# Kernel tuning notes

Measured on AMD Instinct MI355X. Metric: run time of the kernel, lower is better.

## Reference

```python
import jax, jax.numpy as jnp
import numpy as np

# Model dims (match init_kwargs)
N_HEADS = 32
N_KV_HEADS = 8
DIM = 4096
HEAD_DIM = DIM // N_HEADS  # 128
N_REP = N_HEADS // N_KV_HEADS  # 4
MAX_SEQ_LEN = 2048
THETA = 10000.0


def precompute_freqs(dim, end, theta=THETA):
    inv = 1.0 / (theta ** (jnp.arange(0, dim, 2, dtype=jnp.float32) / dim))  # [dim/2]
    t = jnp.arange(end, dtype=jnp.float32)
    f = jnp.outer(t, inv)  # [end, dim/2]
    return jnp.cos(f), jnp.sin(f)


def apply_rope(x, cos, sin):
    # x: [b, s, h, d]; cos/sin: [s, d/2]. Pairs (x[...,2i], x[...,2i+1]) form complex numbers.
    xr = x[..., 0::2]
    xi = x[..., 1::2]
    c = cos[None, :, None, :]
    s = sin[None, :, None, :]
    out_r = xr * c - xi * s
    out_i = xr * s + xi * c
    return jnp.stack([out_r, out_i], axis=-1).reshape(x.shape)


def setup_inputs() -> dict:
    key = jax.random.key(0)
    ks = jax.random.split(key, 5)
    B, S = 4, 1024
    x = jax.random.normal(ks[0], (B, S, DIM), dtype=jnp.float32)
    wq = jax.random.normal(ks[1], (DIM, N_HEADS * HEAD_DIM), dtype=jnp.float32) * 0.02
    wk = jax.random.normal(ks[2], (DIM, N_KV_HEADS * HEAD_DIM), dtype=jnp.float32) * 0.02
    wv = jax.random.normal(ks[3], (DIM, N_KV_HEADS * HEAD_DIM), dtype=jnp.float32) * 0.02
    wo = jax.random.normal(ks[4], (N_HEADS * HEAD_DIM, DIM), dtype=jnp.float32) * 0.02
    # causal mask, additive: 0 on/below diagonal, -1e9 above
    mask = jnp.where(jnp.tril(jnp.ones((S, S), dtype=bool)), 0.0, -1e9).astype(jnp.float32)[None, None]
    return {"x": x, "wq": wq, "wk": wk, "wv": wv, "wo": wo, "mask": mask, "start_pos": 0}


def reference(x, wq, wk, wv, wo, mask, start_pos):
    B, S, _ = x.shape
    # QKV projections
    xq = (x @ wq).reshape(B, S, N_HEADS, HEAD_DIM)
    xk = (x @ wk).reshape(B, S, N_KV_HEADS, HEAD_DIM)
    xv = (x @ wv).reshape(B, S, N_KV_HEADS, HEAD_DIM)
    # RoPE on q, k at positions [start_pos, start_pos+S)
    cos, sin = precompute_freqs(HEAD_DIM, MAX_SEQ_LEN * 2)
    cos_s = jax.lax.dynamic_slice_in_dim(cos, start_pos, S, 0)
    sin_s = jax.lax.dynamic_slice_in_dim(sin, start_pos, S, 0)
    xq = apply_rope(xq, cos_s, sin_s)
    xk = apply_rope(xk, cos_s, sin_s)
    # KV-cache scatter-update (cache starts zeroed), then read prefix
    cache_k = jnp.zeros((B, MAX_SEQ_LEN, N_KV_HEADS, HEAD_DIM), dtype=x.dtype)
    cache_v = jnp.zeros_like(cache_k)
    cache_k = jax.lax.dynamic_update_slice(cache_k, xk, (0, start_pos, 0, 0))
    cache_v = jax.lax.dynamic_update_slice(cache_v, xv, (0, start_pos, 0, 0))
    kv_len = start_pos + S
    keys = cache_k[:, :kv_len]    # [b, kv_len, n_kv, d]
    values = cache_v[:, :kv_len]
    # GQA without materializing repeated KV: split q heads into (kv_group, rep)
    q = xq.reshape(B, S, N_KV_HEADS, N_REP, HEAD_DIM)
    scale = 1.0 / jnp.sqrt(jnp.float32(HEAD_DIM)).astype(x.dtype)
    scores = jnp.einsum('bsgrd,btgd->bgrst', q, keys) * scale  # [b, g, r, s, t]
    scores = scores + mask.reshape(1, 1, 1, S, kv_len)
    probs = jax.nn.softmax(scores, axis=-1)
    out = jnp.einsum('bgrst,btgd->bsgrd', probs, values)  # [b, s, g, r, d]
    out = out.reshape(B, S, N_HEADS * HEAD_DIM)
    return out @ wo
```

## Files before the change

kernel.cpp:

```cpp
#include <hip/hip_runtime.h>
#include <hip/hip_bf16.h>
#include <stdint.h>

typedef __bf16 bf16raw;
typedef __attribute__((ext_vector_type(8))) __bf16 bf16x8;
typedef __attribute__((ext_vector_type(4))) float f32x4;

#define DIMD 4096
#define NHEAD 32
#define NKVH 8
#define HD 128
#define SEQ 1024
#define NB 4
#define NTOK 4096
#define NQKV 6144

__device__ __forceinline__ void gload_lds16(const void* gsrc, void* ldst) {
  __builtin_amdgcn_global_load_lds(
      (const __attribute__((address_space(1))) void*)gsrc,
      (__attribute__((address_space(3))) void*)ldst, 16, 0, 0);
}

__global__ void cast_f32_bf16_kernel(const float* __restrict__ src,
                                     __hip_bfloat16* __restrict__ dst, int n) {
  int i = (blockIdx.x * 256 + threadIdx.x) * 8;
  if (i >= n) return;
  f32x4 a = *(const f32x4*)(src + i);
  f32x4 b = *(const f32x4*)(src + i + 4);
  union { bf16x8 v; __hip_bfloat16 e[8]; } o;
#pragma unroll
  for (int j = 0; j < 4; ++j) {
    o.e[j] = __float2bfloat16(a[j]);
    o.e[4 + j] = __float2bfloat16(b[j]);
  }
  *(bf16x8*)(dst + i) = o.v;
}

__global__ void transpose_cast_kernel(const float* __restrict__ src,
                                      __hip_bfloat16* __restrict__ dst,
                                      int K, int N) {
  __shared__ float tile[32][33];
  int n0 = blockIdx.x * 32, k0 = blockIdx.y * 32;
  int tx = threadIdx.x, ty = threadIdx.y;
#pragma unroll
  for (int i = 0; i < 4; ++i)
    tile[ty + 8 * i][tx] = src[(size_t)(k0 + ty + 8 * i) * N + n0 + tx];
  __syncthreads();
#pragma unroll
  for (int i = 0; i < 4; ++i)
    dst[(size_t)(n0 + ty + 8 * i) * K + k0 + tx] =
        __float2bfloat16(tile[tx][ty + 8 * i]);
}

__global__ void rope_table_kernel(float* __restrict__ cosb, float* __restrict__ sinb) {
  int idx = blockIdx.x * 256 + threadIdx.x;
  int s = idx >> 6, j = idx & 63;
  float inv = 1.0f / powf(10000.0f, (float)(2 * j) * (1.0f / 128.0f));
  float ang = (float)s * inv;
  cosb[idx] = cosf(ang);
  sinb[idx] = sinf(ang);
}


#define LGSB()                                       \
  asm volatile("s_waitcnt lgkmcnt(0)" ::: "memory"); \
  __builtin_amdgcn_sched_barrier(0)

#define QMFMA(AFR, BFR, MB, NB)                                            \
  _Pragma("unroll") for (int mf2 = 0; mf2 < 4; ++mf2)                      \
  _Pragma("unroll") for (int nf2 = 0; nf2 < 2; ++nf2)                      \
  _Pragma("unroll") for (int kk2 = 0; kk2 < 2; ++kk2)                      \
      acc[(MB) + mf2][(NB) + nf2] = __builtin_amdgcn_mfma_f32_16x16x32_bf16( \
          AFR[mf2 * 2 + kk2], BFR[nf2 * 2 + kk2], acc[(MB) + mf2][(NB) + nf2], 0, 0, 0)

#define TILE4(BUF, ST1, ST2, ST3, ST4, VM)                        \
  {                                                               \
    _Pragma("unroll") for (int mf = 0; mf < 4; ++mf)              \
    _Pragma("unroll") for (int kk = 0; kk < 2; ++kk)              \
        alo[mf * 2 + kk] = ldsA(BUF, mf, kk);                     \
    _Pragma("unroll") for (int nf = 0; nf < 2; ++nf)              \
    _Pragma("unroll") for (int kk = 0; kk < 2; ++kk)              \
        bq[nf * 2 + kk] = ldsB(BUF, nf, kk);                      \
    ST1;                                                          \
    LGSB();                                                       \
    __builtin_amdgcn_s_setprio(1);                                \
    QMFMA(alo, bq, 0, 0);                                         \
    __builtin_amdgcn_s_setprio(0);                                \
    _Pragma("unroll") for (int mf = 0; mf < 4; ++mf)              \
    _Pragma("unroll") for (int kk = 0; kk < 2; ++kk)              \
        ahi[mf * 2 + kk] = ldsA(BUF, mf + 4, kk);                 \
    ST2;                                                          \
    LGSB();                                                       \
    __builtin_amdgcn_s_setprio(1);                                \
    QMFMA(ahi, bq, 4, 0);                                         \
    __builtin_amdgcn_s_setprio(0);                                \
    _Pragma("unroll") for (int nf = 0; nf < 2; ++nf)              \
    _Pragma("unroll") for (int kk = 0; kk < 2; ++kk)              \
        bq[nf * 2 + kk] = ldsB(BUF, nf + 2, kk);                  \
    LGSB();                                                       \
    __builtin_amdgcn_s_setprio(1);                                \
    QMFMA(alo, bq, 0, 2);                                         \
    __builtin_amdgcn_s_setprio(0);                                \
    __builtin_amdgcn_s_barrier();   \
    ST3;                                                          \
    ST4;                                                          \
    __builtin_amdgcn_s_setprio(1);                                \
    QMFMA(ahi, bq, 4, 2);                                         \
    __builtin_amdgcn_s_setprio(0);                                \
    VM;                                                           \
    __builtin_amdgcn_s_barrier();   \
  }

template <typename OutT, bool ROPE>
__global__ __launch_bounds__(512, 2) void gemm256_kernel(
    const __hip_bfloat16* __restrict__ A, const __hip_bfloat16* __restrict__ BT,
    OutT* __restrict__ C, int M, int N, int K,
    const float* __restrict__ cosb, const float* __restrict__ sinb,
    __hip_bfloat16* __restrict__ vtc) {
  __shared__ __align__(16) char lds_[131072];
  const int tid = threadIdx.x;
  const int w = tid >> 6, l = tid & 63;
  const int lr = l & 15, lk = l >> 4;
  const int wm = w >> 2, wn = w & 3;

  const int nbn = N >> 8;
  const int nwg = (M >> 8) * nbn;
  const int cpx = nwg >> 3;
  const int bid = blockIdx.x;
  const int swz = (bid & 7) * cpx + (bid >> 3);
  const int m0 = (swz / nbn) << 8;
  const int n0 = (swz % nbn) << 8;

  const size_t Kb = (size_t)K * 2;
  const char* Ab = (const char*)A + (size_t)m0 * Kb;
  const char* Bb = (const char*)BT + (size_t)n0 * Kb;
  const int srcb = ((l & 7) ^ (l >> 3)) * 16;
  const int crow = l >> 3;

  auto stageA = [&](int buf, int half, int kt) {
#pragma unroll
    for (int j = 0; j < 2; ++j) {
      int row = half * 128 + (w * 2 + j) * 8 + crow;
      gload_lds16(Ab + (size_t)row * Kb + (size_t)kt * 128 + srcb,
                  lds_ + buf * 65536 + half * 16384 + (w * 2 + j) * 1024);
    }
  };
  auto stageB = [&](int buf, int half, int kt) {
#pragma unroll
    for (int j = 0; j < 2; ++j) {
      int row = half * 128 + (w * 2 + j) * 8 + crow;
      gload_lds16(Bb + (size_t)row * Kb + (size_t)kt * 128 + srcb,
                  lds_ + buf * 65536 + 32768 + half * 16384 + (w * 2 + j) * 1024);
    }
  };
  auto ldsA = [&](int buf, int mf, int kk) {
    int rih = mf * 16 + lr;
    int cb = (kk * 64 + lk * 16) ^ ((lr & 7) << 4);
    return *(const bf16x8*)(lds_ + buf * 65536 + wm * 16384 + rih * 128 + cb);
  };
  auto ldsB = [&](int buf, int nf, int kk) {
    int rih = (wn & 1) * 64 + nf * 16 + lr;
    int cb = (kk * 64 + lk * 16) ^ ((lr & 7) << 4);
    return *(const bf16x8*)(lds_ + buf * 65536 + 32768 + (wn >> 1) * 16384 +
                            rih * 128 + cb);
  };

  f32x4 acc[8][4] = {};
  bf16x8 alo[8], ahi[8], bq[4];

  stageA(0, 0, 0);
  stageA(0, 1, 0);
  stageB(0, 0, 0);
  stageB(0, 1, 0);
  stageA(1, 0, 1);
  stageA(1, 1, 1);
  asm volatile("s_waitcnt vmcnt(4)" ::: "memory");
  __builtin_amdgcn_s_barrier();

  const int NT = K >> 6;
  for (int E = 0; E < NT - 2; E += 2) {
    TILE4(0, stageB(1, 0, E + 1), stageB(1, 1, E + 1),
          stageA(0, 0, E + 2), stageA(0, 1, E + 2),
          asm volatile("s_waitcnt vmcnt(4)" ::: "memory"));
    TILE4(1, stageB(0, 0, E + 2), stageB(0, 1, E + 2),
          stageA(1, 0, E + 3), stageA(1, 1, E + 3),
          asm volatile("s_waitcnt vmcnt(4)" ::: "memory"));
  }
  TILE4(0, stageB(1, 0, NT - 1), stageB(1, 1, NT - 1), (void)0, (void)0,
        asm volatile("s_waitcnt vmcnt(0)" ::: "memory"));
  TILE4(1, (void)0, (void)0, (void)0, (void)0, (void)0);

#pragma unroll
  for (int mf = 0; mf < 8; ++mf) {
    int row = m0 + wm * 128 + mf * 16 + lk * 4;
#pragma unroll
    for (int nf = 0; nf < 4; ++nf) {
      int colb = n0 + wn * 64 + nf * 16;
      f32x4 v = acc[mf][nf];
      if constexpr (ROPE) {
        if (colb < 5120) {
          int d = (colb & 127) + lr;
          int jj = d >> 1;
          bool even = (d & 1) == 0;
#pragma unroll
          for (int j = 0; j < 4; ++j) {
            float p = __shfl_xor(v[j], 1);
            int s = (row + j) & (SEQ - 1);
            float c = cosb[s * 64 + jj];
            float sn = sinb[s * 64 + jj];
            v[j] = even ? (v[j] * c - p * sn) : (p * sn + v[j] * c);
          }
        } else {
          int col = colb + lr;
          int d = col & 127;
          int hk = (col >> 7) & 7;
          int b = row >> 10;
          int s = row & (SEQ - 1);
          union { uint64_t u; __hip_bfloat16 e[4]; } pk;
#pragma unroll
          for (int j = 0; j < 4; ++j) pk.e[j] = __float2bfloat16(v[j]);
          size_t off = ((size_t)((b * 8 + hk) * 16 + (s >> 6)) * 128 + d) * 64 +
                       (s & 63);
          *(uint64_t*)(vtc + off) = pk.u;
          continue;
        }
      }
#pragma unroll
      for (int j = 0; j < 4; ++j) {
        size_t off = (size_t)(row + j) * N + colb + lr;
        if constexpr (sizeof(OutT) == 2)
          C[off] = __float2bfloat16(v[j]);
        else
          C[off] = v[j];
      }
    }
  }
}

__global__ __launch_bounds__(256, 2) void attn_kernel(
    const __hip_bfloat16* __restrict__ qkv,
    const __hip_bfloat16* __restrict__ vtc,
    __hip_bfloat16* __restrict__ out) {
  __shared__ __align__(16) char Ks[2][16384];
  __shared__ __align__(16) char Vs[2][16384];
  __shared__ __align__(16) char Ps[4][2048];

  const int tid = threadIdx.x;
  const int w = tid >> 6, l = tid & 63;
  const int lr = l & 15, lk = l >> 4;
  const int bx = blockIdx.x;
  const int pair = bx >> 7;
  const int hb = bx & 127;
  const int h = hb & 31;
  const int b = hb >> 5;
  const int hk = h >> 2;

  const char* KgB = (const char*)qkv +
                    ((size_t)(b * SEQ) * NQKV + DIMD + hk * HD) * 2;
  const char* VgB = (const char*)vtc + (size_t)(b * NKVH + hk) * (16 * 16384);
  char* Pw = &Ps[w][0];

  const float cs = 0.12752039889171495f;
  const float ebias = 11.541560327111707f;

  auto stageK = [&](int buf, int kvb) {
#pragma unroll
    for (int j = 0; j < 4; ++j) {
      int i = w * 4 + j;
      int row = i * 4 + (l >> 4);
      int si = ((l & 15) * 16) ^ ((row & 7) << 4);
      gload_lds16(KgB + (size_t)(kvb + row) * (NQKV * 2) + si,
                  &Ks[buf][i * 1024]);
    }
  };
  auto stageV = [&](int buf, int t) {
#pragma unroll
    for (int j = 0; j < 4; ++j) {
      int i = w * 4 + j;
      int row = i * 8 + (l >> 3);
      int si = ((l & 7) * 16) ^ ((row & 7) << 4);
      gload_lds16(VgB + (size_t)t * 16384 + row * 128 + si,
                  &Vs[buf][i * 1024]);
    }
  };

  for (int qsel = 0; qsel < 2; ++qsel) {
    const int qtile = qsel ? (15 - pair) : pair;
    const int qbase = qtile * 64 + w * 16;
    const int nkv = qtile + 1;

    const __hip_bfloat16* Qp =
        qkv + (size_t)(b * SEQ + qbase + lr) * NQKV + h * HD + lk * 8;
    bf16x8 aq[4];
#pragma unroll
    for (int ks = 0; ks < 4; ++ks) aq[ks] = *(const bf16x8*)(Qp + ks * 32);

    f32x4 O[8] = {};
    float lsum[4] = {0.f, 0.f, 0.f, 0.f};

    stageK(0, 0);
    stageV(0, 0);
    asm volatile("s_waitcnt vmcnt(0)" ::: "memory");
    __syncthreads();

    for (int t = 0; t < nkv; ++t) {
      const int cur = t & 1;
      if (t + 1 < nkv) {
        stageK(cur ^ 1, (t + 1) * 64);
        stageV(cur ^ 1, t + 1);
      }
      const int kvb = t * 64;

      f32x4 st[4] = {};
      __builtin_amdgcn_s_setprio(1);
#pragma unroll
      for (int nt = 0; nt < 4; ++nt) {
        int row = nt * 16 + lr;
        const char* kr = &Ks[cur][row * 256];
        int sw = (row & 7) << 4;
#pragma unroll
        for (int ks = 0; ks < 4; ++ks) {
          bf16x8 bk = *(const bf16x8*)(kr + ((ks * 64 + lk * 16) ^ sw));
          st[nt] = __builtin_amdgcn_mfma_f32_16x16x32_bf16(aq[ks], bk, st[nt], 0, 0, 0);
        }
      }
      __builtin_amdgcn_s_setprio(0);

      const bool needmask = (kvb + 63 > qbase);
#pragma unroll
      for (int j = 0; j < 4; ++j) {
        int qrow = qbase + lk * 4 + j;
        int prow = lk * 4 + j;
        int sw = (prow & 7) << 4;
#pragma unroll
        for (int nt = 0; nt < 4; ++nt) {
          float p = exp2f(fmaf(st[nt][j], cs, -ebias));
          if (needmask && (kvb + nt * 16 + lr > qrow)) p = 0.f;
          lsum[j] += p;
          *(__hip_bfloat16*)(Pw + prow * 128 + (((nt * 16 + lr) * 2) ^ sw)) =
              __float2bfloat16(p);
        }
      }

      asm volatile("s_waitcnt lgkmcnt(0)" ::: "memory");
      __builtin_amdgcn_sched_barrier(0);

      __builtin_amdgcn_s_setprio(1);
#pragma unroll
      for (int ks = 0; ks < 2; ++ks) {
        bf16x8 ap = *(const bf16x8*)(Pw + lr * 128 +
                                     ((ks * 64 + lk * 16) ^ ((lr & 7) << 4)));
#pragma unroll
        for (int dt = 0; dt < 8; ++dt) {
          int row = dt * 16 + lr;
          bf16x8 bv = *(const bf16x8*)(&Vs[cur][row * 128 +
                                               ((ks * 64 + lk * 16) ^ ((row & 7) << 4))]);
          O[dt] = __builtin_amdgcn_mfma_f32_16x16x32_bf16(ap, bv, O[dt], 0, 0, 0);
        }
      }
      __builtin_amdgcn_s_setprio(0);

      __syncthreads();
    }

#pragma unroll
    for (int j = 0; j < 4; ++j) {
      float rs = lsum[j];
      rs += __shfl_xor(rs, 1);
      rs += __shfl_xor(rs, 2);
      rs += __shfl_xor(rs, 4);
      rs += __shfl_xor(rs, 8);
      float inv = 1.0f / rs;
      __hip_bfloat16* orow =
          out + (size_t)(b * SEQ + qbase + lk * 4 + j) * DIMD + h * HD;
#pragma unroll
      for (int dt = 0; dt < 8; ++dt)
        orow[dt * 16 + lr] = __float2bfloat16(O[dt][j] * inv);
    }
  }
}

extern "C" void kernel_launch(void* const* d_in, const int* in_sizes, int n_in,
                              void* d_out, int out_size, void* d_ws, size_t ws_size,
                              hipStream_t stream) {
  const float* x = (const float*)d_in[0];
  const float* wq = (const float*)d_in[1];
  const float* wk = (const float*)d_in[2];
  const float* wv = (const float*)d_in[3];
  const float* wo = (const float*)d_in[4];
  float* out = (float*)d_out;

  char* ws = (char*)d_ws;
  const size_t MB = 1024 * 1024;
  __hip_bfloat16* xb = (__hip_bfloat16*)(ws);
  __hip_bfloat16* wqkvt = (__hip_bfloat16*)(ws + 32 * MB);
  __hip_bfloat16* wot = (__hip_bfloat16*)(ws + 80 * MB);
  __hip_bfloat16* qkv = (__hip_bfloat16*)(ws + 112 * MB);
  __hip_bfloat16* vtc = (__hip_bfloat16*)(ws + 160 * MB);
  float* cosb = (float*)(ws + 168 * MB);
  float* sinb = cosb + SEQ * 64;

  cast_f32_bf16_kernel<<<NTOK * DIMD / 8 / 256, 256, 0, stream>>>(x, xb, NTOK * DIMD);
  transpose_cast_kernel<<<dim3(128, 128), dim3(32, 8), 0, stream>>>(wq, wqkvt, 4096, 4096);
  transpose_cast_kernel<<<dim3(32, 128), dim3(32, 8), 0, stream>>>(
      wk, wqkvt + (size_t)4096 * 4096, 4096, 1024);
  transpose_cast_kernel<<<dim3(32, 128), dim3(32, 8), 0, stream>>>(
      wv, wqkvt + (size_t)5120 * 4096, 4096, 1024);
  transpose_cast_kernel<<<dim3(128, 128), dim3(32, 8), 0, stream>>>(wo, wot, 4096, 4096);
  rope_table_kernel<<<SEQ * 64 / 256, 256, 0, stream>>>(cosb, sinb);
  gemm256_kernel<__hip_bfloat16, true><<<dim3(384), 512, 0, stream>>>(
      xb, wqkvt, qkv, NTOK, NQKV, DIMD, cosb, sinb, vtc);
  attn_kernel<<<dim3(1024), 256, 0, stream>>>(qkv, vtc, xb);
  gemm256_kernel<float, false><<<dim3(256), 512, 0, stream>>>(
      xb, wot, out, NTOK, DIMD, DIMD, nullptr, nullptr, nullptr);
}
```

Baseline: 481.0 us.

## Share K/V tiles across all four GQA heads per block and merge weight transposes

The attention kernel now runs 512-thread blocks in which 8 waves cover the 4 query heads of one KV group and two 32-row query halves. Each K/V tile staged into LDS is therefore reused by four heads instead of being reloaded per head, and each wave processes two 16-row query groups so every loaded K/V fragment feeds twice as many MFMAs. This cuts global K/V traffic and LDS loads per FLOP at the cost of more registers (doubled accumulators) and fewer, larger blocks (256), which may reduce occupancy and load balance. Separately, the Q/K/V weight transposes are merged into one launch and the transpose store is widened to 4-element packed writes.

```diff
diff --git a/kernel.cpp b/kernel.cpp
--- a/kernel.cpp
+++ b/kernel.cpp
@@ -36,20 +36,44 @@
   *(bf16x8*)(dst + i) = o.v;
 }
 
-__global__ void transpose_cast_kernel(const float* __restrict__ src,
-                                      __hip_bfloat16* __restrict__ dst,
-                                      int K, int N) {
+__global__ void transpose_qkv_kernel(const float* __restrict__ wq,
+                                     const float* __restrict__ wk,
+                                     const float* __restrict__ wv,
+                                     __hip_bfloat16* __restrict__ dst) {
+  __shared__ float tile[32][33];
+  int n0 = blockIdx.x * 32;
+  int k0 = blockIdx.y * 32;
+  const float* src;
+  int scol, nsw;
+  if (n0 < 4096) { src = wq; scol = n0; nsw = 4096; }
+  else if (n0 < 5120) { src = wk; scol = n0 - 4096; nsw = 1024; }
+  else { src = wv; scol = n0 - 5120; nsw = 1024; }
+  int tx = threadIdx.x, ty = threadIdx.y;
+#pragma unroll
+  for (int i = 0; i < 4; ++i)
+    tile[ty + 8 * i][tx] = src[(size_t)(k0 + ty + 8 * i) * nsw + scol + tx];
+  __syncthreads();
+  union { ushort4 u; __hip_bfloat16 e[4]; } pk;
+#pragma unroll
+  for (int jj = 0; jj < 4; ++jj)
+    pk.e[jj] = __float2bfloat16(tile[ty * 4 + jj][tx]);
+  *(ushort4*)(dst + (size_t)(n0 + tx) * 4096 + k0 + ty * 4) = pk.u;
+}
+
+__global__ void transpose_wo_kernel(const float* __restrict__ src,
+                                    __hip_bfloat16* __restrict__ dst) {
   __shared__ float tile[32][33];
   int n0 = blockIdx.x * 32, k0 = blockIdx.y * 32;
   int tx = threadIdx.x, ty = threadIdx.y;
 #pragma unroll
   for (int i = 0; i < 4; ++i)
-    tile[ty + 8 * i][tx] = src[(size_t)(k0 + ty + 8 * i) * N + n0 + tx];
+    tile[ty + 8 * i][tx] = src[(size_t)(k0 + ty + 8 * i) * 4096 + n0 + tx];
   __syncthreads();
-#pragma unroll
-  for (int i = 0; i < 4; ++i)
-    dst[(size_t)(n0 + ty + 8 * i) * K + k0 + tx] =
-        __float2bfloat16(tile[tx][ty + 8 * i]);
+  union { ushort4 u; __hip_bfloat16 e[4]; } pk;
+#pragma unroll
+  for (int jj = 0; jj < 4; ++jj)
+    pk.e[jj] = __float2bfloat16(tile[ty * 4 + jj][tx]);
+  *(ushort4*)(dst + (size_t)(n0 + tx) * 4096 + k0 + ty * 4) = pk.u;
 }
 
 __global__ void rope_table_kernel(float* __restrict__ cosb, float* __restrict__ sinb) {
@@ -237,23 +261,24 @@
   }
 }
 
-__global__ __launch_bounds__(256, 2) void attn_kernel(
+__global__ __launch_bounds__(512, 2) void attn_kernel(
     const __hip_bfloat16* __restrict__ qkv,
     const __hip_bfloat16* __restrict__ vtc,
     __hip_bfloat16* __restrict__ out) {
   __shared__ __align__(16) char Ks[2][16384];
   __shared__ __align__(16) char Vs[2][16384];
-  __shared__ __align__(16) char Ps[4][2048];
+  __shared__ __align__(16) char Ps[8][4096];
 
   const int tid = threadIdx.x;
   const int w = tid >> 6, l = tid & 63;
   const int lr = l & 15, lk = l >> 4;
   const int bx = blockIdx.x;
-  const int pair = bx >> 7;
-  const int hb = bx & 127;
-  const int h = hb & 31;
-  const int b = hb >> 5;
-  const int hk = h >> 2;
+  const int p = bx >> 5;
+  const int bh = bx & 31;
+  const int b = bh >> 3;
+  const int hk = bh & 7;
+  const int h = hk * 4 + (w & 3);
+  const int qh = w >> 2;
 
   const char* KgB = (const char*)qkv +
                     ((size_t)(b * SEQ) * NQKV + DIMD + hk * HD) * 2;
@@ -265,38 +290,41 @@
 
   auto stageK = [&](int buf, int kvb) {
 #pragma unroll
-    for (int j = 0; j < 4; ++j) {
-      int i = w * 4 + j;
-      int row = i * 4 + (l >> 4);
+    for (int j = 0; j < 2; ++j) {
+      int i2 = w * 2 + j;
+      int row = i2 * 4 + (l >> 4);
       int si = ((l & 15) * 16) ^ ((row & 7) << 4);
       gload_lds16(KgB + (size_t)(kvb + row) * (NQKV * 2) + si,
-                  &Ks[buf][i * 1024]);
+                  &Ks[buf][i2 * 1024]);
     }
   };
   auto stageV = [&](int buf, int t) {
 #pragma unroll
-    for (int j = 0; j < 4; ++j) {
-      int i = w * 4 + j;
-      int row = i * 8 + (l >> 3);
+    for (int j = 0; j < 2; ++j) {
+      int i2 = w * 2 + j;
+      int row = i2 * 8 + (l >> 3);
       int si = ((l & 7) * 16) ^ ((row & 7) << 4);
       gload_lds16(VgB + (size_t)t * 16384 + row * 128 + si,
-                  &Vs[buf][i * 1024]);
+                  &Vs[buf][i2 * 1024]);
     }
   };
 
   for (int qsel = 0; qsel < 2; ++qsel) {
-    const int qtile = qsel ? (15 - pair) : pair;
-    const int qbase = qtile * 64 + w * 16;
+    const int qtile = qsel ? (15 - p) : p;
+    const int qbaseW = qtile * 64 + qh * 32;
     const int nkv = qtile + 1;
 
-    const __hip_bfloat16* Qp =
-        qkv + (size_t)(b * SEQ + qbase + lr) * NQKV + h * HD + lk * 8;
-    bf16x8 aq[4];
-#pragma unroll
-    for (int ks = 0; ks < 4; ++ks) aq[ks] = *(const bf16x8*)(Qp + ks * 32);
-
-    f32x4 O[8] = {};
-    float lsum[4] = {0.f, 0.f, 0.f, 0.f};
+    bf16x8 aq[8];
+#pragma unroll
+    for (int qg = 0; qg < 2; ++qg) {
+      const __hip_bfloat16* Qp =
+          qkv + (size_t)(b * SEQ + qbaseW + qg * 16 + lr) * NQKV + h * HD + lk * 8;
+#pragma unroll
+      for (int ks = 0; ks < 4; ++ks) aq[qg * 4 + ks] = *(const bf16x8*)(Qp + ks * 32);
+    }
+
+    f32x4 O[16] = {};
+    float lsum[8] = {0.f, 0.f, 0.f, 0.f, 0.f, 0.f, 0.f, 0.f};
 
     stageK(0, 0);
     stageV(0, 0);
@@ -311,34 +339,42 @@
       }
       const int kvb = t * 64;
 
-      f32x4 st[4] = {};
+      f32x4 st[8] = {};
       __builtin_amdgcn_s_setprio(1);
 #pragma unroll
       for (int nt = 0; nt < 4; ++nt) {
         int row = nt * 16 + lr;
         const char* kr = &Ks[cur][row * 256];
         int sw = (row & 7) << 4;
-#pragma unroll
-        for (int ks = 0; ks < 4; ++ks) {
-          bf16x8 bk = *(const bf16x8*)(kr + ((ks * 64 + lk * 16) ^ sw));
-          st[nt] = __builtin_amdgcn_mfma_f32_16x16x32_bf16(aq[ks], bk, st[nt], 0, 0, 0);
-        }
+        bf16x8 bk[4];
+#pragma unroll
+        for (int ks = 0; ks < 4; ++ks)
+          bk[ks] = *(const bf16x8*)(kr + ((ks * 64 + lk * 16) ^ sw));
+#pragma unroll
+        for (int qg = 0; qg < 2; ++qg)
+#pragma unroll
+          for (int ks = 0; ks < 4; ++ks)
+            st[qg * 4 + nt] = __builtin_amdgcn_mfma_f32_16x16x32_bf16(
+                aq[qg * 4 + ks], bk[ks], st[qg * 4 + nt], 0, 0, 0);
       }
       __builtin_amdgcn_s_setprio(0);
 
-      const bool needmask = (kvb + 63 > qbase);
-#pragma unroll
-      for (int j = 0; j < 4; ++j) {
-        int qrow = qbase + lk * 4 + j;
-        int prow = lk * 4 + j;
-        int sw = (prow & 7) << 4;
-#pragma unroll
-        for (int nt = 0; nt < 4; ++nt) {
-          float p = exp2f(fmaf(st[nt][j], cs, -ebias));
-          if (needmask && (kvb + nt * 16 + lr > qrow)) p = 0.f;
-          lsum[j] += p;
-          *(__hip_bfloat16*)(Pw + prow * 128 + (((nt * 16 + lr) * 2) ^ sw)) =
-              __float2bfloat16(p);
+#pragma unroll
+      for (int qg = 0; qg < 2; ++qg) {
+        const bool needmask = (kvb + 63 > qbaseW + qg * 16);
+#pragma unroll
+        for (int j = 0; j < 4; ++j) {
+          int qrow = qbaseW + qg * 16 + lk * 4 + j;
+          int prow = lk * 4 + j;
+          int sw = (prow & 7) << 4;
+#pragma unroll
+          for (int nt = 0; nt < 4; ++nt) {
+            float pv = exp2f(fmaf(st[qg * 4 + nt][j], cs, -ebias));
+            if (needmask && (kvb + nt * 16 + lr > qrow)) pv = 0.f;
+            lsum[qg * 4 + j] += pv;
+            *(__hip_bfloat16*)(Pw + qg * 2048 + prow * 128 +
+                               (((nt * 16 + lr) * 2) ^ sw)) = __float2bfloat16(pv);
+          }
         }
       }
 
@@ -348,14 +384,20 @@
       __builtin_amdgcn_s_setprio(1);
 #pragma unroll
       for (int ks = 0; ks < 2; ++ks) {
-        bf16x8 ap = *(const bf16x8*)(Pw + lr * 128 +
-                                     ((ks * 64 + lk * 16) ^ ((lr & 7) << 4)));
+        bf16x8 ap[2];
+#pragma unroll
+        for (int qg = 0; qg < 2; ++qg)
+          ap[qg] = *(const bf16x8*)(Pw + qg * 2048 + lr * 128 +
+                                    ((ks * 64 + lk * 16) ^ ((lr & 7) << 4)));
 #pragma unroll
         for (int dt = 0; dt < 8; ++dt) {
           int row = dt * 16 + lr;
           bf16x8 bv = *(const bf16x8*)(&Vs[cur][row * 128 +
                                                ((ks * 64 + lk * 16) ^ ((row & 7) << 4))]);
-          O[dt] = __builtin_amdgcn_mfma_f32_16x16x32_bf16(ap, bv, O[dt], 0, 0, 0);
+#pragma unroll
+          for (int qg = 0; qg < 2; ++qg)
+            O[qg * 8 + dt] = __builtin_amdgcn_mfma_f32_16x16x32_bf16(
+                ap[qg], bv, O[qg * 8 + dt], 0, 0, 0);
         }
       }
       __builtin_amdgcn_s_setprio(0);
@@ -364,18 +406,21 @@
     }
 
 #pragma unroll
-    for (int j = 0; j < 4; ++j) {
-      float rs = lsum[j];
-      rs += __shfl_xor(rs, 1);
-      rs += __shfl_xor(rs, 2);
-      rs += __shfl_xor(rs, 4);
-      rs += __shfl_xor(rs, 8);
-      float inv = 1.0f / rs;
-      __hip_bfloat16* orow =
-          out + (size_t)(b * SEQ + qbase + lk * 4 + j) * DIMD + h * HD;
-#pragma unroll
-      for (int dt = 0; dt < 8; ++dt)
-        orow[dt * 16 + lr] = __float2bfloat16(O[dt][j] * inv);
+    for (int qg = 0; qg < 2; ++qg) {
+#pragma unroll
+      for (int j = 0; j < 4; ++j) {
+        float rs = lsum[qg * 4 + j];
+        rs += __shfl_xor(rs, 1);
+        rs += __shfl_xor(rs, 2);
+        rs += __shfl_xor(rs, 4);
+        rs += __shfl_xor(rs, 8);
+        float inv = 1.0f / rs;
+        __hip_bfloat16* orow =
+            out + (size_t)(b * SEQ + qbaseW + qg * 16 + lk * 4 + j) * DIMD + h * HD;
+#pragma unroll
+        for (int dt = 0; dt < 8; ++dt)
+          orow[dt * 16 + lr] = __float2bfloat16(O[qg * 8 + dt][j] * inv);
+      }
     }
   }
 }
@@ -401,16 +446,12 @@
   float* sinb = cosb + SEQ * 64;
 
   cast_f32_bf16_kernel<<<NTOK * DIMD / 8 / 256, 256, 0, stream>>>(x, xb, NTOK * DIMD);
-  transpose_cast_kernel<<<dim3(128, 128), dim3(32, 8), 0, stream>>>(wq, wqkvt, 4096, 4096);
-  transpose_cast_kernel<<<dim3(32, 128), dim3(32, 8), 0, stream>>>(
-      wk, wqkvt + (size_t)4096 * 4096, 4096, 1024);
-  transpose_cast_kernel<<<dim3(32, 128), dim3(32, 8), 0, stream>>>(
-      wv, wqkvt + (size_t)5120 * 4096, 4096, 1024);
-  transpose_cast_kernel<<<dim3(128, 128), dim3(32, 8), 0, stream>>>(wo, wot, 4096, 4096);
+  transpose_qkv_kernel<<<dim3(192, 128), dim3(32, 8), 0, stream>>>(wq, wk, wv, wqkvt);
+  transpose_wo_kernel<<<dim3(128, 128), dim3(32, 8), 0, stream>>>(wo, wot);
   rope_table_kernel<<<SEQ * 64 / 256, 256, 0, stream>>>(cosb, sinb);
   gemm256_kernel<__hip_bfloat16, true><<<dim3(384), 512, 0, stream>>>(
       xb, wqkvt, qkv, NTOK, NQKV, DIMD, cosb, sinb, vtc);
-  attn_kernel<<<dim3(1024), 256, 0, stream>>>(qkv, vtc, xb);
+  attn_kernel<<<dim3(256), 512, 0, stream>>>(qkv, vtc, xb);
   gemm256_kernel<float, false><<<dim3(256), 512, 0, stream>>>(
       xb, wot, out, NTOK, DIMD, DIMD, nullptr, nullptr, nullptr);
 }
```

Result: faster. 468.7 us (-2.6%).
